# Kernel optimization log

Hardware: AMD Instinct MI355X
Metric: run time of the kernel (lower is better)

## Reference

```python
import jax, jax.numpy as jnp
import numpy as np

N_HEAD = 8
D_MODEL = 512
D_QKV = 64
LN_EPS = 1e-6


def setup_inputs() -> dict:
    key = jax.random.key(0)
    ks = jax.random.split(key, 10)
    B, S = 4, 2048
    q = jax.random.normal(ks[0], (B, S, D_MODEL), dtype=jnp.float32)
    k = jax.random.normal(ks[1], (B, S, D_MODEL), dtype=jnp.float32)
    v = jax.random.normal(ks[2], (B, S, D_MODEL), dtype=jnp.float32)
    mask = jax.random.randint(ks[3], (B, S, S), 0, 2, dtype=jnp.int32)
    scale = 1.0 / np.sqrt(D_MODEL)
    Wq = jax.random.normal(ks[4], (D_MODEL, N_HEAD * D_QKV), dtype=jnp.float32) * scale
    Wk = jax.random.normal(ks[5], (D_MODEL, N_HEAD * D_QKV), dtype=jnp.float32) * scale
    Wv = jax.random.normal(ks[6], (D_MODEL, N_HEAD * D_QKV), dtype=jnp.float32) * scale
    Wfc = jax.random.normal(ks[7], (N_HEAD * D_QKV, D_MODEL), dtype=jnp.float32) * scale
    gamma = jnp.ones((D_MODEL,), dtype=jnp.float32)
    beta = jnp.zeros((D_MODEL,), dtype=jnp.float32)
    return {"q": q, "k": k, "v": v, "mask": mask, "Wq": Wq, "Wk": Wk,
            "Wv": Wv, "Wfc": Wfc, "gamma": gamma, "beta": beta}


def _layer_norm(x, gamma, beta):
    mu = jnp.mean(x, axis=-1, keepdims=True)
    var = jnp.mean(jnp.square(x - mu), axis=-1, keepdims=True)
    return (x - mu) * jax.lax.rsqrt(var + LN_EPS) * gamma + beta


def reference(q, k, v, mask, Wq, Wk, Wv, Wfc, gamma, beta):
    B, Sq, _ = q.shape
    Sk = k.shape[1]
    residual = q
    qn = _layer_norm(q, gamma, beta)
    # projections -> [B, S, H, Dk]
    qh = (qn @ Wq).reshape(B, Sq, N_HEAD, D_QKV)
    kh = (k @ Wk).reshape(B, Sk, N_HEAD, D_QKV)
    vh = (v @ Wv).reshape(B, Sk, N_HEAD, D_QKV)
    temp = jnp.float32(D_QKV ** 0.5)
    # scores: [B, H, Sq, Sk]
    attn = jnp.einsum('bqhd,bkhd->bhqk', qh / temp, kh)
    attn = jnp.where(mask[:, None, :, :] == 0, jnp.float32(-1e9), attn)
    attn = jax.nn.softmax(attn, axis=-1)
    out = jnp.einsum('bhqk,bkhd->bqhd', attn, vh).reshape(B, Sq, N_HEAD * D_QKV)
    out = out @ Wfc
    return out + residual
```

## Files before the change

### kernel.cpp

```cpp
#include <hip/hip_runtime.h>

#define BATCH 4
#define SEQ   2048
#define NHEAD 8
#define DQKV  64
#define DMODEL 512
#define ROWS  (BATCH*SEQ)
#define BH    (BATCH*NHEAD)
#define HSTRIDE (SEQ*DQKV)

using f32x4  = __attribute__((ext_vector_type(4))) float;
using short8 = __attribute__((ext_vector_type(8))) short;
using short4v = __attribute__((ext_vector_type(4))) short;

#define MFMA16(a,b,c) __builtin_amdgcn_mfma_f32_16x16x32_bf16((a),(b),(c),0,0,0)

__device__ inline short f2bf(float f) {
    unsigned u = __float_as_uint(f);
    u += 0x7FFFu + ((u >> 16) & 1u);
    return (short)(u >> 16);
}

__global__ __launch_bounds__(256) void ln_cast_kernel(
        const float* __restrict__ q, const float* __restrict__ gamma,
        const float* __restrict__ beta, short* __restrict__ qn) {
    int wave = threadIdx.x >> 6;
    int lane = threadIdx.x & 63;
    int row  = blockIdx.x * 4 + wave;
    const float4* qr = (const float4*)(q + (size_t)row * DMODEL);
    float4 x0 = qr[lane * 2];
    float4 x1 = qr[lane * 2 + 1];
    float s  = x0.x + x0.y + x0.z + x0.w + x1.x + x1.y + x1.z + x1.w;
    float s2 = x0.x*x0.x + x0.y*x0.y + x0.z*x0.z + x0.w*x0.w
             + x1.x*x1.x + x1.y*x1.y + x1.z*x1.z + x1.w*x1.w;
    #pragma unroll
    for (int m = 1; m < 64; m <<= 1) {
        s  += __shfl_xor(s,  m);
        s2 += __shfl_xor(s2, m);
    }
    float mu  = s * (1.0f / DMODEL);
    float var = s2 * (1.0f / DMODEL) - mu * mu;
    float rstd = rsqrtf(var + 1e-6f);
    const float4* g = (const float4*)gamma;
    const float4* be = (const float4*)beta;
    float4 g0 = g[lane*2], g1 = g[lane*2+1];
    float4 b0 = be[lane*2], b1 = be[lane*2+1];
    short8 o;
    o[0] = f2bf((x0.x - mu) * rstd * g0.x + b0.x);
    o[1] = f2bf((x0.y - mu) * rstd * g0.y + b0.y);
    o[2] = f2bf((x0.z - mu) * rstd * g0.z + b0.z);
    o[3] = f2bf((x0.w - mu) * rstd * g0.w + b0.w);
    o[4] = f2bf((x1.x - mu) * rstd * g1.x + b1.x);
    o[5] = f2bf((x1.y - mu) * rstd * g1.y + b1.y);
    o[6] = f2bf((x1.z - mu) * rstd * g1.z + b1.z);
    o[7] = f2bf((x1.w - mu) * rstd * g1.w + b1.w);
    ((short8*)(qn + (size_t)row * DMODEL))[lane] = o;
}

__global__ __launch_bounds__(256) void cast_kv_kernel(
        const float* __restrict__ k, const float* __restrict__ v,
        short* __restrict__ kb, short* __restrict__ vb) {
    const float* src = blockIdx.y ? v : k;
    short* dst = blockIdx.y ? vb : kb;
    size_t i = ((size_t)blockIdx.x * 256 + threadIdx.x) * 8;
    float4 a = *(const float4*)(src + i);
    float4 b = *(const float4*)(src + i + 4);
    short8 o;
    o[0]=f2bf(a.x); o[1]=f2bf(a.y); o[2]=f2bf(a.z); o[3]=f2bf(a.w);
    o[4]=f2bf(b.x); o[5]=f2bf(b.y); o[6]=f2bf(b.z); o[7]=f2bf(b.w);
    *(short8*)(dst + i) = o;
}

__global__ __launch_bounds__(256) void castWT4_kernel(
        const float* __restrict__ W0, const float* __restrict__ W1,
        const float* __restrict__ W2, const float* __restrict__ W3,
        short* __restrict__ T0, short* __restrict__ T1,
        short* __restrict__ T2, short* __restrict__ T3) {
    __shared__ short tile[64 * 68];
    int w = blockIdx.z;
    const float* W = w==0 ? W0 : w==1 ? W1 : w==2 ? W2 : W3;
    short* T = w==0 ? T0 : w==1 ? T1 : w==2 ? T2 : T3;
    int ti = blockIdx.x, tj = blockIdx.y;
    int tid = threadIdx.x;
    #pragma unroll
    for (int p = 0; p < 4; ++p) {
        int idx = tid + p * 256;
        int kl = idx >> 4, c4 = idx & 15;
        float4 f = *(const float4*)(W + (size_t)(tj*64 + kl) * DMODEL + ti*64 + c4*4);
        short4v s; s[0]=f2bf(f.x); s[1]=f2bf(f.y); s[2]=f2bf(f.z); s[3]=f2bf(f.w);
        *(short4v*)(tile + kl*68 + c4*4) = s;
    }
    __syncthreads();
    #pragma unroll
    for (int p = 0; p < 4; ++p) {
        int idx = tid + p * 256;
        int nl = idx >> 4, kseg = idx & 15;
        short4v s;
        #pragma unroll
        for (int i = 0; i < 4; ++i) s[i] = tile[(kseg*4 + i)*68 + nl];
        *(short4v*)(T + (size_t)(ti*64 + nl) * DMODEL + tj*64 + kseg*4) = s;
    }
}

__global__ __launch_bounds__(256) void maskbits_kernel(
        const int* __restrict__ mask, unsigned long long* __restrict__ mbits) {
    size_t gtid = (size_t)blockIdx.x * 256 + threadIdx.x;
    int m = mask[gtid];
    unsigned long long b = __ballot(m != 0);
    if ((threadIdx.x & 63) == 0) mbits[gtid >> 6] = b;
}

__global__ __launch_bounds__(256, 4) void proj_qkv_kernel(
        const short* __restrict__ qn, const short* __restrict__ kb,
        const short* __restrict__ vb,
        const short* __restrict__ Wqt, const short* __restrict__ Wkt,
        const short* __restrict__ Wvt,
        short* __restrict__ qhp, short* __restrict__ khp, short* __restrict__ vhp) {
    __shared__ short Wl[2 * 64 * 72];
    int tid = threadIdx.x, wave = tid >> 6, lane = tid & 63;
    int lm = lane & 15, lg = lane >> 4;
    int which = blockIdx.y >> 3;
    int CB0 = (blockIdx.y & 7) * 64;
    const short* A  = which==0 ? qn  : which==1 ? kb  : vb;
    const short* Wt = which==0 ? Wqt : which==1 ? Wkt : Wvt;
    short* outh     = which==0 ? qhp : which==1 ? khp : vhp;
    float scale = which==0 ? 0.18033688f : 1.0f;

    int RBw = blockIdx.x * 128 + wave * 32;
    int scol = tid >> 2, sseg = tid & 3;
    const short* Wrow = Wt + (size_t)(CB0 + scol) * DMODEL;
    const short* Arow0 = A + (size_t)(RBw + lm) * DMODEL;
    const short* Arow1 = A + (size_t)(RBw + 16 + lm) * DMODEL;

    short8 a[2][2];
    a[0][0] = *(const short8*)(Arow0 + lg * 8);
    a[0][1] = *(const short8*)(Arow0 + 32 + lg * 8);
    a[1][0] = *(const short8*)(Arow1 + lg * 8);
    a[1][1] = *(const short8*)(Arow1 + 32 + lg * 8);
    {
        short8 w0 = ((const short8*)Wrow)[sseg], w1 = ((const short8*)Wrow)[sseg + 4];
        short8* wd = (short8*)(Wl + scol * 72);
        wd[sseg] = w0; wd[sseg + 4] = w1;
    }
    __syncthreads();

    f32x4 acc[2][4] = {};
    for (int kk = 0; kk < DMODEL; kk += 64) {
        int cur = (kk >> 6) & 1;
        bool more = (kk + 64) < DMODEL;
        short8 an[2][2], w0n, w1n;
        if (more) {
            an[0][0] = *(const short8*)(Arow0 + kk + 64 + lg * 8);
            an[0][1] = *(const short8*)(Arow0 + kk + 96 + lg * 8);
            an[1][0] = *(const short8*)(Arow1 + kk + 64 + lg * 8);
            an[1][1] = *(const short8*)(Arow1 + kk + 96 + lg * 8);
            w0n = ((const short8*)(Wrow + kk + 64))[sseg];
            w1n = ((const short8*)(Wrow + kk + 64))[sseg + 4];
        }
        const short* Wc = Wl + cur * 4608;
        #pragma unroll
        for (int cg = 0; cg < 4; ++cg) {
            short8 b0 = *(const short8*)(Wc + (cg*16 + lm) * 72 + lg * 8);
            short8 b1 = *(const short8*)(Wc + (cg*16 + lm) * 72 + 32 + lg * 8);
            #pragma unroll
            for (int rg = 0; rg < 2; ++rg) {
                acc[rg][cg] = MFMA16(a[rg][0], b0, acc[rg][cg]);
                acc[rg][cg] = MFMA16(a[rg][1], b1, acc[rg][cg]);
            }
        }
        if (more) {
            #pragma unroll
            for (int rg = 0; rg < 2; ++rg) { a[rg][0] = an[rg][0]; a[rg][1] = an[rg][1]; }
            short8* wd = (short8*)(Wl + (cur ^ 1) * 4608 + scol * 72);
            wd[sseg] = w0n; wd[sseg + 4] = w1n;
        }
        __syncthreads();
    }

    #pragma unroll
    for (int rg = 0; rg < 2; ++rg) {
        #pragma unroll
        for (int cg = 0; cg < 4; ++cg) {
            int n = CB0 + cg * 16 + lm;
            int h = n >> 6, d = n & 63;
            #pragma unroll
            for (int r = 0; r < 4; ++r) {
                int m = RBw + rg * 16 + lg * 4 + r;
                int bb = m >> 11, s = m & 2047;
                outh[(size_t)(bb * NHEAD + h) * HSTRIDE + (size_t)s * DQKV + d] =
                    f2bf(acc[rg][cg][r] * scale);
            }
        }
    }
}

__global__ __launch_bounds__(256) void vtrans_kernel(
        const short* __restrict__ vh, short* __restrict__ vt) {
    __shared__ short t[64 * 68];
    int st = blockIdx.x, bh = blockIdx.y;
    int s0 = st * 64;
    int tid = threadIdx.x;
    const short* src = vh + (size_t)bh * HSTRIDE + (size_t)s0 * DQKV;
    #pragma unroll
    for (int p = 0; p < 2; ++p) {
        int idx = tid + p * 256;
        int sl = idx >> 3, seg = idx & 7;
        short8 val = *(const short8*)(src + (size_t)sl * DQKV + seg * 8);
        short4v lo = {val[0], val[1], val[2], val[3]};
        short4v hi = {val[4], val[5], val[6], val[7]};
        *(short4v*)(t + sl*68 + seg*8)     = lo;
        *(short4v*)(t + sl*68 + seg*8 + 4) = hi;
    }
    __syncthreads();
    short* dst = vt + (size_t)bh * HSTRIDE + s0;
    #pragma unroll
    for (int p = 0; p < 2; ++p) {
        int idx = tid + p * 256;
        int d = idx >> 3, sseg = idx & 7;
        short8 o;
        #pragma unroll
        for (int i = 0; i < 8; ++i) o[i] = t[(sseg*8 + i)*68 + d];
        *(short8*)(dst + (size_t)d * SEQ + sseg * 8) = o;
    }
}

#define KL_OFF 0
#define VL_OFF 9216
#define PW_OFF 18576
__global__ __launch_bounds__(256, 3) void attn_kernel(
        const short* __restrict__ qh, const short* __restrict__ kh,
        const short* __restrict__ vt, const unsigned long long* __restrict__ mbits,
        short* __restrict__ oh) {
    __shared__ short lds[27280];
    int tid = threadIdx.x, wave = tid >> 6, lane = tid & 63;
    int lm = lane & 15, lg = lane >> 4;
    int qt = blockIdx.x, bh = blockIdx.y;
    int b = bh >> 3;
    int qbase = qt * 128 + wave * 32;
    short* Pw = lds + PW_OFF + wave * 2176;

    const short* Kbase = kh + (size_t)bh * HSTRIDE;
    const short* Vtb   = vt + (size_t)bh * HSTRIDE;

    short8 aq[2][2];
    #pragma unroll
    for (int rg = 0; rg < 2; ++rg) {
        const short8* Qrow = (const short8*)(qh + (size_t)bh * HSTRIDE
                              + (size_t)(qbase + rg * 16 + lm) * DQKV);
        aq[rg][0] = Qrow[lg];
        aq[rg][1] = Qrow[lg + 4];
    }

    if (tid < 128) lds[VL_OFF + (tid >> 6) * 4680 + 64 * 72 + (tid & 63)] = (short)0x3F80;

    f32x4 o[2][4] = {};
    f32x4 ox[2] = {};

    int skey = tid >> 2, sseg = tid & 3;
    const unsigned long long* mb = mbits + ((size_t)(b * SEQ + qbase) << 5)
                                   + (size_t)lg * 128;

    {
        const short8* Ks = (const short8*)(Kbase + (size_t)skey * DQKV);
        short8 k0 = Ks[sseg], k1 = Ks[sseg + 4];
        const short* Vs = Vtb + (size_t)skey * SEQ;
        short8 v0 = *(const short8*)(Vs + sseg * 8);
        short8 v1 = *(const short8*)(Vs + sseg * 8 + 32);
        short8* kd = (short8*)(lds + KL_OFF + skey * 72);
        kd[sseg] = k0; kd[sseg + 4] = k1;
        *(short8*)(lds + VL_OFF + skey * 72 + sseg * 8)      = v0;
        *(short8*)(lds + VL_OFF + skey * 72 + sseg * 8 + 32) = v1;
    }
    __syncthreads();

    for (int kt = 0; kt < SEQ; kt += 64) {
        int cur = (kt >> 6) & 1;
        bool more = (kt + 64) < SEQ;
        short8 nk0, nk1, nv0, nv1;
        if (more) {
            const short8* Ks = (const short8*)(Kbase + (size_t)(kt + 64 + skey) * DQKV);
            nk0 = Ks[sseg]; nk1 = Ks[sseg + 4];
            const short* Vs = Vtb + (size_t)skey * SEQ + kt + 64;
            nv0 = *(const short8*)(Vs + sseg * 8);
            nv1 = *(const short8*)(Vs + sseg * 8 + 32);
        }

        const short* Kc = lds + KL_OFF + cur * 4608;
        f32x4 sk[2][4];
        #pragma unroll
        for (int kg = 0; kg < 4; ++kg) {
            short8 bk0 = *(const short8*)(Kc + (kg*16 + lm) * 72 + lg * 8);
            short8 bk1 = *(const short8*)(Kc + (kg*16 + lm) * 72 + 32 + lg * 8);
            #pragma unroll
            for (int rg = 0; rg < 2; ++rg) {
                f32x4 z{};
                z = MFMA16(aq[rg][0], bk0, z);
                sk[rg][kg] = MFMA16(aq[rg][1], bk1, z);
            }
        }

        int w64 = kt >> 6;
        #pragma unroll
        for (int rg = 0; rg < 2; ++rg) {
            #pragma unroll
            for (int r = 0; r < 4; ++r) {
                unsigned long long msk = mb[rg * 512 + r * 32 + w64] >> lm;
                short* pdst = Pw + (rg * 16 + lg * 4 + r) * 68 + lm;
                #pragma unroll
                for (int kg = 0; kg < 4; ++kg) {
                    float e = __builtin_amdgcn_exp2f(sk[rg][kg][r]);
                    float p = ((unsigned)(msk >> (kg * 16)) & 1u) ? e : 0.0f;
                    pdst[kg * 16] = (short)(__float_as_uint(p) >> 16);
                }
            }
        }

        short8 ap[2][2];
        #pragma unroll
        for (int rg = 0; rg < 2; ++rg) {
            const short* pr = Pw + (rg * 16 + lm) * 68;
            short4v l0 = *(const short4v*)(pr + lg * 8);
            short4v h0 = *(const short4v*)(pr + lg * 8 + 4);
            short4v l1 = *(const short4v*)(pr + 32 + lg * 8);
            short4v h1 = *(const short4v*)(pr + 32 + lg * 8 + 4);
            ap[rg][0] = __builtin_shufflevector(l0, h0, 0,1,2,3,4,5,6,7);
            ap[rg][1] = __builtin_shufflevector(l1, h1, 0,1,2,3,4,5,6,7);
        }

        const short* Vc = lds + VL_OFF + cur * 4680;
        #pragma unroll
        for (int dt = 0; dt < 4; ++dt) {
            short8 bv0 = *(const short8*)(Vc + (dt*16 + lm) * 72 + lg * 8);
            short8 bv1 = *(const short8*)(Vc + (dt*16 + lm) * 72 + 32 + lg * 8);
            #pragma unroll
            for (int rg = 0; rg < 2; ++rg) {
                o[rg][dt] = MFMA16(ap[rg][0], bv0, o[rg][dt]);
                o[rg][dt] = MFMA16(ap[rg][1], bv1, o[rg][dt]);
            }
        }
        {
            short8 bx0 = *(const short8*)(Vc + (64 + lm) * 72 + lg * 8);
            short8 bx1 = *(const short8*)(Vc + (64 + lm) * 72 + 32 + lg * 8);
            #pragma unroll
            for (int rg = 0; rg < 2; ++rg) {
                ox[rg] = MFMA16(ap[rg][0], bx0, ox[rg]);
                ox[rg] = MFMA16(ap[rg][1], bx1, ox[rg]);
            }
        }

        if (more) {
            int nxt = cur ^ 1;
            short8* kd = (short8*)(lds + KL_OFF + nxt * 4608 + skey * 72);
            kd[sseg] = nk0; kd[sseg + 4] = nk1;
            *(short8*)(lds + VL_OFF + nxt * 4680 + skey * 72 + sseg * 8)      = nv0;
            *(short8*)(lds + VL_OFF + nxt * 4680 + skey * 72 + sseg * 8 + 32) = nv1;
        }
        __syncthreads();
    }

    short* ob = oh + (size_t)bh * HSTRIDE;
    #pragma unroll
    for (int rg = 0; rg < 2; ++rg) {
        float rinv[4];
        #pragma unroll
        for (int r = 0; r < 4; ++r)
            rinv[r] = __builtin_amdgcn_rcpf(__shfl(ox[rg][r], lane & 48));
        #pragma unroll
        for (int dt = 0; dt < 4; ++dt) {
            #pragma unroll
            for (int r = 0; r < 4; ++r) {
                ob[(size_t)(qbase + rg * 16 + lg * 4 + r) * DQKV + dt * 16 + lm] =
                    f2bf(o[rg][dt][r] * rinv[r]);
            }
        }
    }
}

__global__ __launch_bounds__(256, 4) void outproj_kernel(
        const short* __restrict__ Ah, const short* __restrict__ Wfct,
        const float* __restrict__ resid, float* __restrict__ out) {
    __shared__ short Wl[2 * 64 * 72];
    int tid = threadIdx.x, wave = tid >> 6, lane = tid & 63;
    int lm = lane & 15, lg = lane >> 4;
    int CB0 = blockIdx.y * 64;
    int RBw = blockIdx.x * 128 + wave * 32;
    int scol = tid >> 2, sseg = tid & 3;
    const short* Wrow = Wfct + (size_t)(CB0 + scol) * DMODEL;

    size_t rb[2];
    #pragma unroll
    for (int rg = 0; rg < 2; ++rg) {
        int m = RBw + rg * 16 + lm;
        rb[rg] = (size_t)(m >> 11) * (NHEAD * HSTRIDE) + (size_t)(m & 2047) * DQKV;
    }

    short8 a[2][2];
    #pragma unroll
    for (int rg = 0; rg < 2; ++rg) {
        a[rg][0] = *(const short8*)(Ah + rb[rg] + lg * 8);
        a[rg][1] = *(const short8*)(Ah + rb[rg] + 32 + lg * 8);
    }
    {
        short8 w0 = ((const short8*)Wrow)[sseg], w1 = ((const short8*)Wrow)[sseg + 4];
        short8* wd = (short8*)(Wl + scol * 72);
        wd[sseg] = w0; wd[sseg + 4] = w1;
    }
    __syncthreads();

    f32x4 acc[2][4] = {};
    for (int kk = 0; kk < DMODEL; kk += 64) {
        int cur = (kk >> 6) & 1;
        bool more = (kk + 64) < DMODEL;
        short8 an[2][2], w0n, w1n;
        if (more) {
            size_t hoff = (size_t)((kk >> 6) + 1) * HSTRIDE;
            #pragma unroll
            for (int rg = 0; rg < 2; ++rg) {
                an[rg][0] = *(const short8*)(Ah + rb[rg] + hoff + lg * 8);
                an[rg][1] = *(const short8*)(Ah + rb[rg] + hoff + 32 + lg * 8);
            }
            w0n = ((const short8*)(Wrow + kk + 64))[sseg];
            w1n = ((const short8*)(Wrow + kk + 64))[sseg + 4];
        }
        const short* Wc = Wl + cur * 4608;
        #pragma unroll
        for (int cg = 0; cg < 4; ++cg) {
            short8 b0 = *(const short8*)(Wc + (cg*16 + lm) * 72 + lg * 8);
            short8 b1 = *(const short8*)(Wc + (cg*16 + lm) * 72 + 32 + lg * 8);
            #pragma unroll
            for (int rg = 0; rg < 2; ++rg) {
                acc[rg][cg] = MFMA16(a[rg][0], b0, acc[rg][cg]);
                acc[rg][cg] = MFMA16(a[rg][1], b1, acc[rg][cg]);
            }
        }
        if (more) {
            #pragma unroll
            for (int rg = 0; rg < 2; ++rg) { a[rg][0] = an[rg][0]; a[rg][1] = an[rg][1]; }
            short8* wd = (short8*)(Wl + (cur ^ 1) * 4608 + scol * 72);
            wd[sseg] = w0n; wd[sseg + 4] = w1n;
        }
        __syncthreads();
    }

    #pragma unroll
    for (int rg = 0; rg < 2; ++rg) {
        #pragma unroll
        for (int cg = 0; cg < 4; ++cg) {
            int n = CB0 + cg * 16 + lm;
            #pragma unroll
            for (int r = 0; r < 4; ++r) {
                int m = RBw + rg * 16 + lg * 4 + r;
                size_t idx = (size_t)m * DMODEL + n;
                out[idx] = acc[rg][cg][r] + resid[idx];
            }
        }
    }
}

extern "C" void kernel_launch(void* const* d_in, const int* in_sizes, int n_in,
                              void* d_out, int out_size, void* d_ws, size_t ws_size,
                              hipStream_t stream) {
    const float* q     = (const float*)d_in[0];
    const float* k     = (const float*)d_in[1];
    const float* v     = (const float*)d_in[2];
    const int*   mask  = (const int*)d_in[3];
    const float* Wq    = (const float*)d_in[4];
    const float* Wk    = (const float*)d_in[5];
    const float* Wv    = (const float*)d_in[6];
    const float* Wfc   = (const float*)d_in[7];
    const float* gamma = (const float*)d_in[8];
    const float* beta  = (const float*)d_in[9];
    float* out = (float*)d_out;

    char* ws = (char*)d_ws;
    const size_t SZ_ROWS = (size_t)ROWS * DMODEL * sizeof(short);
    const size_t SZ_W    = (size_t)DMODEL * DMODEL * sizeof(short);
    short* qn   = (short*)(ws);
    short* kbf  = (short*)(ws + SZ_ROWS);
    short* vbf  = (short*)(ws + 2 * SZ_ROWS);
    short* Wqt  = (short*)(ws + 3 * SZ_ROWS);
    short* Wkt  = (short*)(ws + 3 * SZ_ROWS + SZ_W);
    short* Wvt  = (short*)(ws + 3 * SZ_ROWS + 2 * SZ_W);
    short* Wfct = (short*)(ws + 3 * SZ_ROWS + 3 * SZ_W);
    short* qhb  = (short*)(ws + 3 * SZ_ROWS + 4 * SZ_W);
    short* khb  = (short*)(ws + 4 * SZ_ROWS + 4 * SZ_W);
    short* vhb  = (short*)(ws + 5 * SZ_ROWS + 4 * SZ_W);
    unsigned long long* mbits = (unsigned long long*)(ws + 6 * SZ_ROWS + 4 * SZ_W);
    short* vtb  = kbf;
    short* aout = qn;

    ln_cast_kernel<<<ROWS / 4, 256, 0, stream>>>(q, gamma, beta, qn);
    cast_kv_kernel<<<dim3(ROWS * DMODEL / (256 * 8), 2), 256, 0, stream>>>(k, v, kbf, vbf);
    castWT4_kernel<<<dim3(8, 8, 4), 256, 0, stream>>>(Wq, Wk, Wv, Wfc, Wqt, Wkt, Wvt, Wfct);
    maskbits_kernel<<<BATCH * SEQ * SEQ / 256, 256, 0, stream>>>(mask, mbits);

    proj_qkv_kernel<<<dim3(ROWS / 128, 24), 256, 0, stream>>>(
        qn, kbf, vbf, Wqt, Wkt, Wvt, qhb, khb, vhb);

    vtrans_kernel<<<dim3(SEQ / 64, BH), 256, 0, stream>>>(vhb, vtb);

    attn_kernel<<<dim3(SEQ / 128, BH), 256, 0, stream>>>(qhb, khb, vtb, mbits, aout);

    outproj_kernel<<<dim3(ROWS / 128, DMODEL / 64), 256, 0, stream>>>(aout, Wfct, q, out);
}
```

Before: 299.5 us.

## Use direct global-to-LDS loads with XOR swizzle, fuse prep kernels, prepack mask per lane

Merges the LN and K/V cast kernels into one launch. Writes V transposed straight from the projection epilogue, which removes the separate transpose kernel. Replaces register-staged LDS fills with global_load_lds into XOR-swizzled 64x64 tiles for the projection, attention and output-projection GEMMs. Repacks the mask into per-lane ballot words consumed via v_cndmask, and computes row sums with a constant ones operand instead of an extra LDS row. The goal is less LDS padding and bank conflict, fewer register round trips and fewer launches, at the cost of lower attention occupancy (launch bound 2) and a more complex mask-packing pass.

```diff
diff --git a/kernel.cpp b/kernel.cpp
--- a/kernel.cpp
+++ b/kernel.cpp
@@ -15,60 +15,79 @@
 
 #define MFMA16(a,b,c) __builtin_amdgcn_mfma_f32_16x16x32_bf16((a),(b),(c),0,0,0)
 
-__device__ inline short f2bf(float f) {
+__device__ __forceinline__ short f2bf(float f) {
     unsigned u = __float_as_uint(f);
     u += 0x7FFFu + ((u >> 16) & 1u);
     return (short)(u >> 16);
 }
 
-__global__ __launch_bounds__(256) void ln_cast_kernel(
-        const float* __restrict__ q, const float* __restrict__ gamma,
-        const float* __restrict__ beta, short* __restrict__ qn) {
-    int wave = threadIdx.x >> 6;
-    int lane = threadIdx.x & 63;
-    int row  = blockIdx.x * 4 + wave;
-    const float4* qr = (const float4*)(q + (size_t)row * DMODEL);
-    float4 x0 = qr[lane * 2];
-    float4 x1 = qr[lane * 2 + 1];
-    float s  = x0.x + x0.y + x0.z + x0.w + x1.x + x1.y + x1.z + x1.w;
-    float s2 = x0.x*x0.x + x0.y*x0.y + x0.z*x0.z + x0.w*x0.w
-             + x1.x*x1.x + x1.y*x1.y + x1.z*x1.z + x1.w*x1.w;
-    #pragma unroll
-    for (int m = 1; m < 64; m <<= 1) {
-        s  += __shfl_xor(s,  m);
-        s2 += __shfl_xor(s2, m);
-    }
-    float mu  = s * (1.0f / DMODEL);
-    float var = s2 * (1.0f / DMODEL) - mu * mu;
-    float rstd = rsqrtf(var + 1e-6f);
-    const float4* g = (const float4*)gamma;
-    const float4* be = (const float4*)beta;
-    float4 g0 = g[lane*2], g1 = g[lane*2+1];
-    float4 b0 = be[lane*2], b1 = be[lane*2+1];
-    short8 o;
-    o[0] = f2bf((x0.x - mu) * rstd * g0.x + b0.x);
-    o[1] = f2bf((x0.y - mu) * rstd * g0.y + b0.y);
-    o[2] = f2bf((x0.z - mu) * rstd * g0.z + b0.z);
-    o[3] = f2bf((x0.w - mu) * rstd * g0.w + b0.w);
-    o[4] = f2bf((x1.x - mu) * rstd * g1.x + b1.x);
-    o[5] = f2bf((x1.y - mu) * rstd * g1.y + b1.y);
-    o[6] = f2bf((x1.z - mu) * rstd * g1.z + b1.z);
-    o[7] = f2bf((x1.w - mu) * rstd * g1.w + b1.w);
-    ((short8*)(qn + (size_t)row * DMODEL))[lane] = o;
-}
-
-__global__ __launch_bounds__(256) void cast_kv_kernel(
-        const float* __restrict__ k, const float* __restrict__ v,
-        short* __restrict__ kb, short* __restrict__ vb) {
-    const float* src = blockIdx.y ? v : k;
-    short* dst = blockIdx.y ? vb : kb;
-    size_t i = ((size_t)blockIdx.x * 256 + threadIdx.x) * 8;
-    float4 a = *(const float4*)(src + i);
-    float4 b = *(const float4*)(src + i + 4);
-    short8 o;
-    o[0]=f2bf(a.x); o[1]=f2bf(a.y); o[2]=f2bf(a.z); o[3]=f2bf(a.w);
-    o[4]=f2bf(b.x); o[5]=f2bf(b.y); o[6]=f2bf(b.z); o[7]=f2bf(b.w);
-    *(short8*)(dst + i) = o;
+__device__ __forceinline__ void gl2lds16(const short* g, short* l) {
+    __builtin_amdgcn_global_load_lds(
+        (__attribute__((address_space(1))) void*)g,
+        (__attribute__((address_space(3))) void*)l, 16, 0, 0);
+}
+
+__device__ __forceinline__ void stage64x64(const short* g0, int gstride, short* lt, int t) {
+    #pragma unroll
+    for (int p = 0; p < 2; ++p) {
+        int o = p * 2048 + t * 8;
+        int row = o >> 6;
+        int c = ((o >> 3) & 7) ^ (row & 7);
+        gl2lds16(g0 + (size_t)row * gstride + c * 8, lt + o);
+    }
+}
+
+__device__ __forceinline__ short8 trd(const short* t, int row, int c) {
+    return *(const short8*)(t + row * 64 + ((c ^ (row & 7)) << 3));
+}
+
+__global__ __launch_bounds__(256) void prep_kernel(
+        const float* __restrict__ q, const float* __restrict__ k,
+        const float* __restrict__ v, const float* __restrict__ gamma,
+        const float* __restrict__ beta,
+        short* __restrict__ qn, short* __restrict__ kb, short* __restrict__ vb) {
+    if (blockIdx.y == 0) {
+        int wave = threadIdx.x >> 6, lane = threadIdx.x & 63;
+        int row  = blockIdx.x * 4 + wave;
+        const float4* qr = (const float4*)(q + (size_t)row * DMODEL);
+        float4 x0 = qr[lane * 2];
+        float4 x1 = qr[lane * 2 + 1];
+        float s  = x0.x + x0.y + x0.z + x0.w + x1.x + x1.y + x1.z + x1.w;
+        float s2 = x0.x*x0.x + x0.y*x0.y + x0.z*x0.z + x0.w*x0.w
+                 + x1.x*x1.x + x1.y*x1.y + x1.z*x1.z + x1.w*x1.w;
+        #pragma unroll
+        for (int m = 1; m < 64; m <<= 1) {
+            s  += __shfl_xor(s,  m);
+            s2 += __shfl_xor(s2, m);
+        }
+        float mu  = s * (1.0f / DMODEL);
+        float var = s2 * (1.0f / DMODEL) - mu * mu;
+        float rstd = rsqrtf(var + 1e-6f);
+        const float4* g = (const float4*)gamma;
+        const float4* be = (const float4*)beta;
+        float4 g0 = g[lane*2], g1 = g[lane*2+1];
+        float4 b0 = be[lane*2], b1 = be[lane*2+1];
+        short8 o;
+        o[0] = f2bf((x0.x - mu) * rstd * g0.x + b0.x);
+        o[1] = f2bf((x0.y - mu) * rstd * g0.y + b0.y);
+        o[2] = f2bf((x0.z - mu) * rstd * g0.z + b0.z);
+        o[3] = f2bf((x0.w - mu) * rstd * g0.w + b0.w);
+        o[4] = f2bf((x1.x - mu) * rstd * g1.x + b1.x);
+        o[5] = f2bf((x1.y - mu) * rstd * g1.y + b1.y);
+        o[6] = f2bf((x1.z - mu) * rstd * g1.z + b1.z);
+        o[7] = f2bf((x1.w - mu) * rstd * g1.w + b1.w);
+        ((short8*)(qn + (size_t)row * DMODEL))[lane] = o;
+    } else {
+        const float* src = (blockIdx.y == 1) ? k : v;
+        short* dst = (blockIdx.y == 1) ? kb : vb;
+        size_t i = (size_t)blockIdx.x * 2048 + (size_t)threadIdx.x * 8;
+        float4 a = *(const float4*)(src + i);
+        float4 b = *(const float4*)(src + i + 4);
+        short8 o;
+        o[0]=f2bf(a.x); o[1]=f2bf(a.y); o[2]=f2bf(a.z); o[3]=f2bf(a.w);
+        o[4]=f2bf(b.x); o[5]=f2bf(b.y); o[6]=f2bf(b.z); o[7]=f2bf(b.w);
+        *(short8*)(dst + i) = o;
+    }
 }
 
 __global__ __launch_bounds__(256) void castWT4_kernel(
@@ -102,12 +121,25 @@
     }
 }
 
-__global__ __launch_bounds__(256) void maskbits_kernel(
-        const int* __restrict__ mask, unsigned long long* __restrict__ mbits) {
-    size_t gtid = (size_t)blockIdx.x * 256 + threadIdx.x;
-    int m = mask[gtid];
-    unsigned long long b = __ballot(m != 0);
-    if ((threadIdx.x & 63) == 0) mbits[gtid >> 6] = b;
+__global__ __launch_bounds__(256) void maskpack_kernel(
+        const int* __restrict__ mask, unsigned long long* __restrict__ mp) {
+    int gw = blockIdx.x * 4 + (threadIdx.x >> 6);
+    int lane = threadIdx.x & 63;
+    int r   = gw & 3;
+    int rg  = (gw >> 2) & 1;
+    int w64 = (gw >> 3) & 31;
+    int qg  = (gw >> 8) & 63;
+    int b   = gw >> 14;
+    int row = qg * 32 + rg * 16 + (lane >> 4) * 4 + r;
+    const int* src = mask + ((size_t)b * SEQ + row) * SEQ + w64 * 64 + (lane & 15);
+    unsigned long long w0 = __ballot(src[0]  != 0);
+    unsigned long long w1 = __ballot(src[16] != 0);
+    unsigned long long w2 = __ballot(src[32] != 0);
+    unsigned long long w3 = __ballot(src[48] != 0);
+    if (lane == 0) {
+        unsigned long long* d = mp + (size_t)gw * 4;
+        d[0] = w0; d[1] = w1; d[2] = w2; d[3] = w3;
+    }
 }
 
 __global__ __launch_bounds__(256, 4) void proj_qkv_kernel(
@@ -115,53 +147,46 @@
         const short* __restrict__ vb,
         const short* __restrict__ Wqt, const short* __restrict__ Wkt,
         const short* __restrict__ Wvt,
-        short* __restrict__ qhp, short* __restrict__ khp, short* __restrict__ vhp) {
-    __shared__ short Wl[2 * 64 * 72];
+        short* __restrict__ qhp, short* __restrict__ khp, short* __restrict__ vtp) {
+    __shared__ __align__(16) short Wl[2 * 4096];
     int tid = threadIdx.x, wave = tid >> 6, lane = tid & 63;
     int lm = lane & 15, lg = lane >> 4;
     int which = blockIdx.y >> 3;
     int CB0 = (blockIdx.y & 7) * 64;
     const short* A  = which==0 ? qn  : which==1 ? kb  : vb;
     const short* Wt = which==0 ? Wqt : which==1 ? Wkt : Wvt;
-    short* outh     = which==0 ? qhp : which==1 ? khp : vhp;
     float scale = which==0 ? 0.18033688f : 1.0f;
 
     int RBw = blockIdx.x * 128 + wave * 32;
-    int scol = tid >> 2, sseg = tid & 3;
-    const short* Wrow = Wt + (size_t)(CB0 + scol) * DMODEL;
     const short* Arow0 = A + (size_t)(RBw + lm) * DMODEL;
     const short* Arow1 = A + (size_t)(RBw + 16 + lm) * DMODEL;
+    const short* W0 = Wt + (size_t)CB0 * DMODEL;
 
     short8 a[2][2];
     a[0][0] = *(const short8*)(Arow0 + lg * 8);
     a[0][1] = *(const short8*)(Arow0 + 32 + lg * 8);
     a[1][0] = *(const short8*)(Arow1 + lg * 8);
     a[1][1] = *(const short8*)(Arow1 + 32 + lg * 8);
-    {
-        short8 w0 = ((const short8*)Wrow)[sseg], w1 = ((const short8*)Wrow)[sseg + 4];
-        short8* wd = (short8*)(Wl + scol * 72);
-        wd[sseg] = w0; wd[sseg + 4] = w1;
-    }
+    stage64x64(W0, DMODEL, Wl, tid);
     __syncthreads();
 
     f32x4 acc[2][4] = {};
     for (int kk = 0; kk < DMODEL; kk += 64) {
         int cur = (kk >> 6) & 1;
         bool more = (kk + 64) < DMODEL;
-        short8 an[2][2], w0n, w1n;
+        short8 an[2][2];
         if (more) {
+            stage64x64(W0 + kk + 64, DMODEL, Wl + (cur ^ 1) * 4096, tid);
             an[0][0] = *(const short8*)(Arow0 + kk + 64 + lg * 8);
             an[0][1] = *(const short8*)(Arow0 + kk + 96 + lg * 8);
             an[1][0] = *(const short8*)(Arow1 + kk + 64 + lg * 8);
             an[1][1] = *(const short8*)(Arow1 + kk + 96 + lg * 8);
-            w0n = ((const short8*)(Wrow + kk + 64))[sseg];
-            w1n = ((const short8*)(Wrow + kk + 64))[sseg + 4];
-        }
-        const short* Wc = Wl + cur * 4608;
+        }
+        const short* Wc = Wl + cur * 4096;
         #pragma unroll
         for (int cg = 0; cg < 4; ++cg) {
-            short8 b0 = *(const short8*)(Wc + (cg*16 + lm) * 72 + lg * 8);
-            short8 b1 = *(const short8*)(Wc + (cg*16 + lm) * 72 + 32 + lg * 8);
+            short8 b0 = trd(Wc, cg*16 + lm, lg);
+            short8 b1 = trd(Wc, cg*16 + lm, lg + 4);
             #pragma unroll
             for (int rg = 0; rg < 2; ++rg) {
                 acc[rg][cg] = MFMA16(a[rg][0], b0, acc[rg][cg]);
@@ -171,73 +196,56 @@
         if (more) {
             #pragma unroll
             for (int rg = 0; rg < 2; ++rg) { a[rg][0] = an[rg][0]; a[rg][1] = an[rg][1]; }
-            short8* wd = (short8*)(Wl + (cur ^ 1) * 4608 + scol * 72);
-            wd[sseg] = w0n; wd[sseg + 4] = w1n;
         }
         __syncthreads();
     }
 
-    #pragma unroll
-    for (int rg = 0; rg < 2; ++rg) {
-        #pragma unroll
-        for (int cg = 0; cg < 4; ++cg) {
-            int n = CB0 + cg * 16 + lm;
-            int h = n >> 6, d = n & 63;
-            #pragma unroll
-            for (int r = 0; r < 4; ++r) {
-                int m = RBw + rg * 16 + lg * 4 + r;
-                int bb = m >> 11, s = m & 2047;
-                outh[(size_t)(bb * NHEAD + h) * HSTRIDE + (size_t)s * DQKV + d] =
-                    f2bf(acc[rg][cg][r] * scale);
-            }
-        }
-    }
-}
-
-__global__ __launch_bounds__(256) void vtrans_kernel(
-        const short* __restrict__ vh, short* __restrict__ vt) {
-    __shared__ short t[64 * 68];
-    int st = blockIdx.x, bh = blockIdx.y;
-    int s0 = st * 64;
-    int tid = threadIdx.x;
-    const short* src = vh + (size_t)bh * HSTRIDE + (size_t)s0 * DQKV;
-    #pragma unroll
-    for (int p = 0; p < 2; ++p) {
-        int idx = tid + p * 256;
-        int sl = idx >> 3, seg = idx & 7;
-        short8 val = *(const short8*)(src + (size_t)sl * DQKV + seg * 8);
-        short4v lo = {val[0], val[1], val[2], val[3]};
-        short4v hi = {val[4], val[5], val[6], val[7]};
-        *(short4v*)(t + sl*68 + seg*8)     = lo;
-        *(short4v*)(t + sl*68 + seg*8 + 4) = hi;
-    }
-    __syncthreads();
-    short* dst = vt + (size_t)bh * HSTRIDE + s0;
-    #pragma unroll
-    for (int p = 0; p < 2; ++p) {
-        int idx = tid + p * 256;
-        int d = idx >> 3, sseg = idx & 7;
-        short8 o;
-        #pragma unroll
-        for (int i = 0; i < 8; ++i) o[i] = t[(sseg*8 + i)*68 + d];
-        *(short8*)(dst + (size_t)d * SEQ + sseg * 8) = o;
-    }
-}
-
-#define KL_OFF 0
-#define VL_OFF 9216
-#define PW_OFF 18576
-__global__ __launch_bounds__(256, 3) void attn_kernel(
+    if (which < 2) {
+        short* outh = which==0 ? qhp : khp;
+        #pragma unroll
+        for (int rg = 0; rg < 2; ++rg) {
+            #pragma unroll
+            for (int cg = 0; cg < 4; ++cg) {
+                int n = CB0 + cg * 16 + lm;
+                int h = n >> 6, d = n & 63;
+                #pragma unroll
+                for (int r = 0; r < 4; ++r) {
+                    int m = RBw + rg * 16 + lg * 4 + r;
+                    int bb = m >> 11, s = m & 2047;
+                    outh[(size_t)(bb * NHEAD + h) * HSTRIDE + (size_t)s * DQKV + d] =
+                        f2bf(acc[rg][cg][r] * scale);
+                }
+            }
+        }
+    } else {
+        int bb = RBw >> 11;
+        #pragma unroll
+        for (int rg = 0; rg < 2; ++rg) {
+            int s0 = (RBw + rg * 16 + lg * 4) & 2047;
+            #pragma unroll
+            for (int cg = 0; cg < 4; ++cg) {
+                int n = CB0 + cg * 16 + lm;
+                int h = n >> 6, d = n & 63;
+                short4v pk;
+                #pragma unroll
+                for (int r = 0; r < 4; ++r) pk[r] = f2bf(acc[rg][cg][r]);
+                *(short4v*)(vtp + (size_t)(bb * NHEAD + h) * HSTRIDE
+                            + (size_t)d * SEQ + s0) = pk;
+            }
+        }
+    }
+}
+
+__global__ __launch_bounds__(256, 2) void attn_kernel(
         const short* __restrict__ qh, const short* __restrict__ kh,
-        const short* __restrict__ vt, const unsigned long long* __restrict__ mbits,
+        const short* __restrict__ vt, const unsigned long long* __restrict__ mpack,
         short* __restrict__ oh) {
-    __shared__ short lds[27280];
+    __shared__ __align__(16) short lds[24576];
     int tid = threadIdx.x, wave = tid >> 6, lane = tid & 63;
     int lm = lane & 15, lg = lane >> 4;
-    int qt = blockIdx.x, bh = blockIdx.y;
-    int b = bh >> 3;
+    int qt = blockIdx.x, bh = blockIdx.y, b = bh >> 3;
     int qbase = qt * 128 + wave * 32;
-    short* Pw = lds + PW_OFF + wave * 2176;
+    short* Pw = lds + 16384 + wave * 2048;
 
     const short* Kbase = kh + (size_t)bh * HSTRIDE;
     const short* Vtb   = vt + (size_t)bh * HSTRIDE;
@@ -251,46 +259,34 @@
         aq[rg][1] = Qrow[lg + 4];
     }
 
-    if (tid < 128) lds[VL_OFF + (tid >> 6) * 4680 + 64 * 72 + (tid & 63)] = (short)0x3F80;
+    int qg = __builtin_amdgcn_readfirstlane(qt * 4 + wave);
+    const unsigned long long* mbase = mpack + (size_t)(b * 64 + qg) * 1024;
+
+    const short one = (short)0x3F80;
+    short8 ones = {one, one, one, one, one, one, one, one};
 
     f32x4 o[2][4] = {};
     f32x4 ox[2] = {};
 
-    int skey = tid >> 2, sseg = tid & 3;
-    const unsigned long long* mb = mbits + ((size_t)(b * SEQ + qbase) << 5)
-                                   + (size_t)lg * 128;
-
-    {
-        const short8* Ks = (const short8*)(Kbase + (size_t)skey * DQKV);
-        short8 k0 = Ks[sseg], k1 = Ks[sseg + 4];
-        const short* Vs = Vtb + (size_t)skey * SEQ;
-        short8 v0 = *(const short8*)(Vs + sseg * 8);
-        short8 v1 = *(const short8*)(Vs + sseg * 8 + 32);
-        short8* kd = (short8*)(lds + KL_OFF + skey * 72);
-        kd[sseg] = k0; kd[sseg + 4] = k1;
-        *(short8*)(lds + VL_OFF + skey * 72 + sseg * 8)      = v0;
-        *(short8*)(lds + VL_OFF + skey * 72 + sseg * 8 + 32) = v1;
-    }
+    stage64x64(Kbase, DQKV, lds, tid);
+    stage64x64(Vtb,   SEQ,  lds + 8192, tid);
     __syncthreads();
 
     for (int kt = 0; kt < SEQ; kt += 64) {
         int cur = (kt >> 6) & 1;
-        bool more = (kt + 64) < SEQ;
-        short8 nk0, nk1, nv0, nv1;
-        if (more) {
-            const short8* Ks = (const short8*)(Kbase + (size_t)(kt + 64 + skey) * DQKV);
-            nk0 = Ks[sseg]; nk1 = Ks[sseg + 4];
-            const short* Vs = Vtb + (size_t)skey * SEQ + kt + 64;
-            nv0 = *(const short8*)(Vs + sseg * 8);
-            nv1 = *(const short8*)(Vs + sseg * 8 + 32);
-        }
-
-        const short* Kc = lds + KL_OFF + cur * 4608;
+        if (kt + 64 < SEQ) {
+            int nxt = cur ^ 1;
+            stage64x64(Kbase + (size_t)(kt + 64) * DQKV, DQKV, lds + nxt * 4096, tid);
+            stage64x64(Vtb + kt + 64, SEQ, lds + 8192 + nxt * 4096, tid);
+        }
+        const short* Kc = lds + cur * 4096;
+        const short* Vc = lds + 8192 + cur * 4096;
+
         f32x4 sk[2][4];
         #pragma unroll
         for (int kg = 0; kg < 4; ++kg) {
-            short8 bk0 = *(const short8*)(Kc + (kg*16 + lm) * 72 + lg * 8);
-            short8 bk1 = *(const short8*)(Kc + (kg*16 + lm) * 72 + 32 + lg * 8);
+            short8 bk0 = trd(Kc, kg*16 + lm, lg);
+            short8 bk1 = trd(Kc, kg*16 + lm, lg + 4);
             #pragma unroll
             for (int rg = 0; rg < 2; ++rg) {
                 f32x4 z{};
@@ -299,18 +295,21 @@
             }
         }
 
-        int w64 = kt >> 6;
+        const unsigned long long* mw = mbase + (kt >> 6) * 32;
         #pragma unroll
         for (int rg = 0; rg < 2; ++rg) {
             #pragma unroll
             for (int r = 0; r < 4; ++r) {
-                unsigned long long msk = mb[rg * 512 + r * 32 + w64] >> lm;
-                short* pdst = Pw + (rg * 16 + lg * 4 + r) * 68 + lm;
+                int row = rg * 16 + lg * 4 + r;
+                short* pd = Pw + row * 64 + (lm & 7);
                 #pragma unroll
                 for (int kg = 0; kg < 4; ++kg) {
+                    unsigned long long mword = mw[rg * 16 + r * 4 + kg];
                     float e = __builtin_amdgcn_exp2f(sk[rg][kg][r]);
-                    float p = ((unsigned)(msk >> (kg * 16)) & 1u) ? e : 0.0f;
-                    pdst[kg * 16] = (short)(__float_as_uint(p) >> 16);
+                    float pe;
+                    asm("v_cndmask_b32 %0, 0, %1, %2" : "=v"(pe) : "v"(e), "s"(mword));
+                    int c = (2 * kg + (lm >> 3)) ^ (row & 7);
+                    pd[c * 8] = (short)(__float_as_uint(pe) >> 16);
                 }
             }
         }
@@ -318,42 +317,24 @@
         short8 ap[2][2];
         #pragma unroll
         for (int rg = 0; rg < 2; ++rg) {
-            const short* pr = Pw + (rg * 16 + lm) * 68;
-            short4v l0 = *(const short4v*)(pr + lg * 8);
-            short4v h0 = *(const short4v*)(pr + lg * 8 + 4);
-            short4v l1 = *(const short4v*)(pr + 32 + lg * 8);
-            short4v h1 = *(const short4v*)(pr + 32 + lg * 8 + 4);
-            ap[rg][0] = __builtin_shufflevector(l0, h0, 0,1,2,3,4,5,6,7);
-            ap[rg][1] = __builtin_shufflevector(l1, h1, 0,1,2,3,4,5,6,7);
-        }
-
-        const short* Vc = lds + VL_OFF + cur * 4680;
+            ap[rg][0] = trd(Pw, rg*16 + lm, lg);
+            ap[rg][1] = trd(Pw, rg*16 + lm, lg + 4);
+        }
+
         #pragma unroll
         for (int dt = 0; dt < 4; ++dt) {
-            short8 bv0 = *(const short8*)(Vc + (dt*16 + lm) * 72 + lg * 8);
-            short8 bv1 = *(const short8*)(Vc + (dt*16 + lm) * 72 + 32 + lg * 8);
+            short8 bv0 = trd(Vc, dt*16 + lm, lg);
+            short8 bv1 = trd(Vc, dt*16 + lm, lg + 4);
             #pragma unroll
             for (int rg = 0; rg < 2; ++rg) {
                 o[rg][dt] = MFMA16(ap[rg][0], bv0, o[rg][dt]);
                 o[rg][dt] = MFMA16(ap[rg][1], bv1, o[rg][dt]);
             }
         }
-        {
-            short8 bx0 = *(const short8*)(Vc + (64 + lm) * 72 + lg * 8);
-            short8 bx1 = *(const short8*)(Vc + (64 + lm) * 72 + 32 + lg * 8);
-            #pragma unroll
-            for (int rg = 0; rg < 2; ++rg) {
-                ox[rg] = MFMA16(ap[rg][0], bx0, ox[rg]);
-                ox[rg] = MFMA16(ap[rg][1], bx1, ox[rg]);
-            }
-        }
-
-        if (more) {
-            int nxt = cur ^ 1;
-            short8* kd = (short8*)(lds + KL_OFF + nxt * 4608 + skey * 72);
-            kd[sseg] = nk0; kd[sseg + 4] = nk1;
-            *(short8*)(lds + VL_OFF + nxt * 4680 + skey * 72 + sseg * 8)      = nv0;
-            *(short8*)(lds + VL_OFF + nxt * 4680 + skey * 72 + sseg * 8 + 32) = nv1;
+        #pragma unroll
+        for (int rg = 0; rg < 2; ++rg) {
+            ox[rg] = MFMA16(ap[rg][0], ones, ox[rg]);
+            ox[rg] = MFMA16(ap[rg][1], ones, ox[rg]);
         }
         __syncthreads();
     }
@@ -363,8 +344,7 @@
     for (int rg = 0; rg < 2; ++rg) {
         float rinv[4];
         #pragma unroll
-        for (int r = 0; r < 4; ++r)
-            rinv[r] = __builtin_amdgcn_rcpf(__shfl(ox[rg][r], lane & 48));
+        for (int r = 0; r < 4; ++r) rinv[r] = __builtin_amdgcn_rcpf(ox[rg][r]);
         #pragma unroll
         for (int dt = 0; dt < 4; ++dt) {
             #pragma unroll
@@ -379,13 +359,12 @@
 __global__ __launch_bounds__(256, 4) void outproj_kernel(
         const short* __restrict__ Ah, const short* __restrict__ Wfct,
         const float* __restrict__ resid, float* __restrict__ out) {
-    __shared__ short Wl[2 * 64 * 72];
+    __shared__ __align__(16) short Wl[2 * 4096];
     int tid = threadIdx.x, wave = tid >> 6, lane = tid & 63;
     int lm = lane & 15, lg = lane >> 4;
     int CB0 = blockIdx.y * 64;
     int RBw = blockIdx.x * 128 + wave * 32;
-    int scol = tid >> 2, sseg = tid & 3;
-    const short* Wrow = Wfct + (size_t)(CB0 + scol) * DMODEL;
+    const short* W0 = Wfct + (size_t)CB0 * DMODEL;
 
     size_t rb[2];
     #pragma unroll
@@ -400,33 +379,28 @@
         a[rg][0] = *(const short8*)(Ah + rb[rg] + lg * 8);
         a[rg][1] = *(const short8*)(Ah + rb[rg] + 32 + lg * 8);
     }
-    {
-        short8 w0 = ((const short8*)Wrow)[sseg], w1 = ((const short8*)Wrow)[sseg + 4];
-        short8* wd = (short8*)(Wl + scol * 72);
-        wd[sseg] = w0; wd[sseg + 4] = w1;
-    }
+    stage64x64(W0, DMODEL, Wl, tid);
     __syncthreads();
 
     f32x4 acc[2][4] = {};
     for (int kk = 0; kk < DMODEL; kk += 64) {
         int cur = (kk >> 6) & 1;
         bool more = (kk + 64) < DMODEL;
-        short8 an[2][2], w0n, w1n;
+        short8 an[2][2];
         if (more) {
+            stage64x64(W0 + kk + 64, DMODEL, Wl + (cur ^ 1) * 4096, tid);
             size_t hoff = (size_t)((kk >> 6) + 1) * HSTRIDE;
             #pragma unroll
             for (int rg = 0; rg < 2; ++rg) {
                 an[rg][0] = *(const short8*)(Ah + rb[rg] + hoff + lg * 8);
                 an[rg][1] = *(const short8*)(Ah + rb[rg] + hoff + 32 + lg * 8);
             }
-            w0n = ((const short8*)(Wrow + kk + 64))[sseg];
-            w1n = ((const short8*)(Wrow + kk + 64))[sseg + 4];
-        }
-        const short* Wc = Wl + cur * 4608;
+        }
+        const short* Wc = Wl + cur * 4096;
         #pragma unroll
         for (int cg = 0; cg < 4; ++cg) {
-            short8 b0 = *(const short8*)(Wc + (cg*16 + lm) * 72 + lg * 8);
-            short8 b1 = *(const short8*)(Wc + (cg*16 + lm) * 72 + 32 + lg * 8);
+            short8 b0 = trd(Wc, cg*16 + lm, lg);
+            short8 b1 = trd(Wc, cg*16 + lm, lg + 4);
             #pragma unroll
             for (int rg = 0; rg < 2; ++rg) {
                 acc[rg][cg] = MFMA16(a[rg][0], b0, acc[rg][cg]);
@@ -436,8 +410,6 @@
         if (more) {
             #pragma unroll
             for (int rg = 0; rg < 2; ++rg) { a[rg][0] = an[rg][0]; a[rg][1] = an[rg][1]; }
-            short8* wd = (short8*)(Wl + (cur ^ 1) * 4608 + scol * 72);
-            wd[sseg] = w0n; wd[sseg + 4] = w1n;
         }
         __syncthreads();
     }
@@ -484,22 +456,18 @@
     short* Wfct = (short*)(ws + 3 * SZ_ROWS + 3 * SZ_W);
     short* qhb  = (short*)(ws + 3 * SZ_ROWS + 4 * SZ_W);
     short* khb  = (short*)(ws + 4 * SZ_ROWS + 4 * SZ_W);
-    short* vhb  = (short*)(ws + 5 * SZ_ROWS + 4 * SZ_W);
-    unsigned long long* mbits = (unsigned long long*)(ws + 6 * SZ_ROWS + 4 * SZ_W);
-    short* vtb  = kbf;
+    short* vtb  = (short*)(ws + 5 * SZ_ROWS + 4 * SZ_W);
+    unsigned long long* mpack = (unsigned long long*)(ws + 6 * SZ_ROWS + 4 * SZ_W);
     short* aout = qn;
 
-    ln_cast_kernel<<<ROWS / 4, 256, 0, stream>>>(q, gamma, beta, qn);
-    cast_kv_kernel<<<dim3(ROWS * DMODEL / (256 * 8), 2), 256, 0, stream>>>(k, v, kbf, vbf);
+    prep_kernel<<<dim3(ROWS / 4, 3), 256, 0, stream>>>(q, k, v, gamma, beta, qn, kbf, vbf);
     castWT4_kernel<<<dim3(8, 8, 4), 256, 0, stream>>>(Wq, Wk, Wv, Wfc, Wqt, Wkt, Wvt, Wfct);
-    maskbits_kernel<<<BATCH * SEQ * SEQ / 256, 256, 0, stream>>>(mask, mbits);
+    maskpack_kernel<<<65536 / 4, 256, 0, stream>>>(mask, mpack);
 
     proj_qkv_kernel<<<dim3(ROWS / 128, 24), 256, 0, stream>>>(
-        qn, kbf, vbf, Wqt, Wkt, Wvt, qhb, khb, vhb);
-
-    vtrans_kernel<<<dim3(SEQ / 64, BH), 256, 0, stream>>>(vhb, vtb);
-
-    attn_kernel<<<dim3(SEQ / 128, BH), 256, 0, stream>>>(qhb, khb, vtb, mbits, aout);
+        qn, kbf, vbf, Wqt, Wkt, Wvt, qhb, khb, vtb);
+
+    attn_kernel<<<dim3(SEQ / 128, BH), 256, 0, stream>>>(qhb, khb, vtb, mpack, aout);
 
     outproj_kernel<<<dim3(ROWS / 128, DMODEL / 64), 256, 0, stream>>>(aout, Wfct, q, out);
 }
```

Result: faster. 284.1 us (-5.1%).
